# Optimization experiments

Hardware: AMD Instinct MI355X
Metric: run time of the kernel (lower is better)

The kernel has to match this reference:

```python
import jax, jax.numpy as jnp
import numpy as np

D_MODEL = 768
N_HEAD = 12
N_KV_HEADS = 4
HEAD_DIM = D_MODEL // N_HEAD
N_REPEAT = N_HEAD // N_KV_HEADS
ROPE_BASE = 10000.0


def _rotate_half(x):
    # Faithful to the torch impl: reshape(..., 2, d/2) -> transpose(-2,-1) -> reshape
    # (interleaves the two halves), then chunk and cat(-x2, x1).
    d = x.shape[-1]
    xh = x.reshape(*x.shape[:-1], 2, d // 2).swapaxes(-2, -1).reshape(x.shape)
    x1, x2 = jnp.split(xh, 2, axis=-1)
    return jnp.concatenate([-x2, x1], axis=-1)


def _rope(x, pos):
    # x: [B, h, T, d], pos: [T] int
    d = x.shape[-1]
    inv_freq = 1.0 / (ROPE_BASE ** (jnp.arange(0, d, 2, dtype=jnp.float32) / d))
    freqs = pos.astype(jnp.float32)[:, None] * inv_freq[None, :]      # [T, d/2]
    emb = jnp.concatenate([freqs, freqs], axis=-1)                     # [T, d]
    cos = jnp.cos(emb)[None, None]                                     # [1,1,T,d]
    sin = jnp.sin(emb)[None, None]
    xf = x.astype(jnp.float32)
    return (xf * cos + _rotate_half(xf) * sin).astype(x.dtype)


def setup_inputs() -> dict:
    key = jax.random.key(0)
    ks = jax.random.split(key, 6)
    B, T, C = 8, 1024, D_MODEL
    s = 0.02
    return {
        "x": jax.random.normal(ks[0], (B, T, C), dtype=jnp.float32),
        "pos": jnp.arange(T, dtype=jnp.int32),
        "q_w": jax.random.normal(ks[1], (C, N_HEAD * HEAD_DIM), dtype=jnp.float32) * s,
        "q_b": jnp.zeros((N_HEAD * HEAD_DIM,), dtype=jnp.float32),
        "k_w": jax.random.normal(ks[2], (C, N_KV_HEADS * HEAD_DIM), dtype=jnp.float32) * s,
        "k_b": jnp.zeros((N_KV_HEADS * HEAD_DIM,), dtype=jnp.float32),
        "v_w": jax.random.normal(ks[3], (C, N_KV_HEADS * HEAD_DIM), dtype=jnp.float32) * s,
        "v_b": jnp.zeros((N_KV_HEADS * HEAD_DIM,), dtype=jnp.float32),
        "o_w": jax.random.normal(ks[4], (C, C), dtype=jnp.float32) * s,
        "o_b": jnp.zeros((C,), dtype=jnp.float32),
    }


def reference(x, pos, q_w, q_b, k_w, k_b, v_w, v_b, o_w, o_b):
    B, T, C = x.shape
    hd, H, KVH, rep = HEAD_DIM, N_HEAD, N_KV_HEADS, N_REPEAT

    Q = (x @ q_w + q_b).reshape(B, T, H, hd).transpose(0, 2, 1, 3)     # [B,H,T,hd]
    K = (x @ k_w + k_b).reshape(B, T, KVH, hd).transpose(0, 2, 1, 3)   # [B,KVH,T,hd]
    V = (x @ v_w + v_b).reshape(B, T, KVH, hd).transpose(0, 2, 1, 3)

    Q = _rope(Q, pos)
    K = _rope(K, pos)

    # Grouped attention: avoid materializing repeated KV (equiv. to repeat_interleave).
    Qg = Q.reshape(B, KVH, rep, T, hd)
    scores = jnp.einsum("bgrtd,bgsd->bgrts", Qg, K) / np.sqrt(hd).astype(np.float32)
    causal = jnp.tril(jnp.ones((T, T), dtype=bool))
    scores = jnp.where(causal, scores, jnp.finfo(scores.dtype).min)
    probs = jax.nn.softmax(scores, axis=-1)
    out = jnp.einsum("bgrts,bgsd->bgrtd", probs, V)                    # [B,KVH,rep,T,hd]
    out = out.reshape(B, H, T, hd).transpose(0, 2, 1, 3).reshape(B, T, C)
    return out @ o_w + o_b
```

## Files before the change

kernel.cpp:

```cpp
#include <hip/hip_runtime.h>
#include <hip/hip_bf16.h>
#include <math.h>

#define BATCH 8
#define SEQ   1024
#define DM    768
#define NHEAD 12
#define KVH   4
#define HD    64
#define REP   3

#define QSCALE 0.18033688011112042f

typedef unsigned short u16;
typedef __attribute__((ext_vector_type(8))) __bf16 bf16x8;
typedef __attribute__((ext_vector_type(4))) float f32x4;
typedef __attribute__((ext_vector_type(4))) unsigned int u32x4;
typedef __attribute__((address_space(1))) const unsigned int gu32_c;
typedef __attribute__((address_space(3))) unsigned int su32;

__device__ __forceinline__ u16 f2bf(float f) {
    unsigned int u = __float_as_uint(f);
    u += 0x7fffu + ((u >> 16) & 1u);
    return (u16)(u >> 16);
}

__global__ __launch_bounds__(256) void cvt_x_k(
    const float* __restrict__ in, u16* __restrict__ o, int n4)
{
    const int i = blockIdx.x * 256 + threadIdx.x;
    if (i >= n4) return;
    const float4 v = ((const float4*)in)[i];
    ushort4 r;
    r.x = f2bf(v.x); r.y = f2bf(v.y); r.z = f2bf(v.z); r.w = f2bf(v.w);
    ((ushort4*)o)[i] = r;
}

__global__ __launch_bounds__(256) void cvt_wqkv_k(
    const float* __restrict__ qw, const float* __restrict__ kw,
    const float* __restrict__ vw, u16* __restrict__ wt)
{
    const int idx = blockIdx.x * 256 + threadIdx.x;
    if (idx >= 1280 * DM) return;
    const int k = idx % DM;
    const int n = idx / DM;
    float v;
    if (n < 768)       v = qw[(size_t)k * 768 + n] * QSCALE;
    else if (n < 1024) v = kw[(size_t)k * 256 + (n - 768)];
    else               v = vw[(size_t)k * 256 + (n - 1024)];
    wt[idx] = f2bf(v);
}

__global__ __launch_bounds__(256) void cvt_wo_k(
    const float* __restrict__ ow, u16* __restrict__ wt)
{
    const int idx = blockIdx.x * 256 + threadIdx.x;
    if (idx >= DM * DM) return;
    const int k = idx % DM;
    const int n = idx / DM;
    wt[idx] = f2bf(ow[(size_t)k * DM + n]);
}

__device__ __forceinline__ void gemm128_body(
    const u16* __restrict__ A, const u16* __restrict__ B,
    int m0, int n0, u16 (*As)[4096], u16 (*Bs)[4096], f32x4 acc[4][4])
{
    const int tid  = threadIdx.x;
    const int lane = tid & 63;
    const int wid  = tid >> 6;
    const int wr = wid >> 1, wc = wid & 1;
    const int lo = lane & 15, hi = lane >> 4;

    const f32x4 z = {0.f, 0.f, 0.f, 0.f};
    #pragma unroll
    for (int i = 0; i < 4; i++)
        #pragma unroll
        for (int j = 0; j < 4; j++)
            acc[i][j] = z;

    const int NT = DM / 32;

    #define STAGE_G(kt_, sl_) do {                                            \
        _Pragma("unroll")                                                     \
        for (int r_ = 0; r_ < 2; ++r_) {                                      \
            const int idx_  = r_ * 256 + tid;                                 \
            const int row_  = idx_ >> 2;                                      \
            const int col_  = (idx_ & 3) << 3;                                \
            const int base_ = (r_ * 256 + wid * 64) * 8;                      \
            __builtin_amdgcn_global_load_lds(                                 \
                (gu32_c*)&A[(size_t)(m0 + row_) * DM + (kt_) * 32 + col_],    \
                (su32*)&As[sl_][base_], 16, 0, 0);                            \
            __builtin_amdgcn_global_load_lds(                                 \
                (gu32_c*)&B[(size_t)(n0 + row_) * DM + (kt_) * 32 + col_],    \
                (su32*)&Bs[sl_][base_], 16, 0, 0);                            \
        }                                                                     \
    } while (0)

    STAGE_G(0, 0);
    STAGE_G(1, 1);

    for (int kt = 0; kt < NT; ++kt) {
        const int k2 = (kt + 2 < NT) ? kt + 2 : NT - 1;
        STAGE_G(k2, (kt + 2) & 3);
        asm volatile("s_waitcnt vmcnt(8)" ::: "memory");
        __builtin_amdgcn_s_barrier();
        __builtin_amdgcn_sched_barrier(0);

        const int sl = kt & 3;
        bf16x8 af[4], bfr[4];
        #pragma unroll
        for (int i = 0; i < 4; i++) af[i]  = *(const bf16x8*)&As[sl][(wr * 64 + i * 16 + lo) * 32 + hi * 8];
        #pragma unroll
        for (int j = 0; j < 4; j++) bfr[j] = *(const bf16x8*)&Bs[sl][(wc * 64 + j * 16 + lo) * 32 + hi * 8];
        #pragma unroll
        for (int i = 0; i < 4; i++)
            #pragma unroll
            for (int j = 0; j < 4; j++)
                acc[i][j] = __builtin_amdgcn_mfma_f32_16x16x32_bf16(af[i], bfr[j], acc[i][j], 0, 0, 0);
    }
    #undef STAGE_G
}

__global__ __launch_bounds__(256) void gemm_qkv(
    const u16* __restrict__ xb, const u16* __restrict__ wt,
    const float* __restrict__ qb, const float* __restrict__ kb,
    const float* __restrict__ vb,
    u16* __restrict__ Q, u16* __restrict__ K, u16* __restrict__ Vr)
{
    __shared__ __align__(16) u16 As[4][4096];
    __shared__ __align__(16) u16 Bs[4][4096];
    const int id = (blockIdx.x & 7) * 80 + (blockIdx.x >> 3);
    const int m0 = (id / 10) * 128;
    const int n0 = (id % 10) * 128;
    f32x4 acc[4][4];
    gemm128_body(xb, wt, m0, n0, As, Bs, acc);

    const int tid = threadIdx.x;
    const int lane = tid & 63, wid = tid >> 6;
    const int wr = wid >> 1, wc = wid & 1;
    const int lo = lane & 15, hi = lane >> 4;

    #pragma unroll
    for (int j = 0; j < 4; j++) {
        const int n = n0 + wc * 64 + j * 16 + lo;
        u16* outp; int nl, Hcnt; float bias;
        if (n < 768)       { outp = Q;  nl = n;        Hcnt = NHEAD; bias = qb[n] * QSCALE; }
        else if (n < 1024) { outp = K;  nl = n - 768;  Hcnt = KVH;   bias = kb[nl]; }
        else               { outp = Vr; nl = n - 1024; Hcnt = KVH;   bias = vb[nl]; }
        const int head = nl >> 6, d = nl & 63;
        #pragma unroll
        for (int i = 0; i < 4; i++) {
            #pragma unroll
            for (int r = 0; r < 4; r++) {
                const int m = m0 + wr * 64 + i * 16 + hi * 4 + r;
                const int b = m >> 10, t = m & 1023;
                outp[(((size_t)(b * Hcnt + head)) * SEQ + t) * HD + d] =
                    f2bf(acc[i][j][r] + bias);
            }
        }
    }
}

__global__ __launch_bounds__(256) void vtrans_k(
    const u16* __restrict__ in, u16* __restrict__ out)
{
    __shared__ u16 T[64][72];
    const int blk = blockIdx.x;
    const int bg  = blk >> 4;
    const int t0  = (blk & 15) << 6;
    const int tid = threadIdx.x;
    const int tl  = tid & 63;
    const int d0  = (tid >> 6) << 4;

    union { u32x4 v[2]; u16 u[16]; } ld;
    const u16* src = in + ((size_t)bg * SEQ + t0 + tl) * HD + d0;
    ld.v[0] = *(const u32x4*)(src);
    ld.v[1] = *(const u32x4*)(src + 8);
    #pragma unroll
    for (int k = 0; k < 16; ++k) T[d0 + k][tl] = ld.u[k];
    __syncthreads();

    const int d  = tid >> 2;
    const int tc = (tid & 3) << 4;
    u16* dst = out + ((size_t)bg * HD + d) * SEQ + t0 + tc;
    *(u32x4*)(dst)     = *(const u32x4*)&T[d][tc];
    *(u32x4*)(dst + 8) = *(const u32x4*)&T[d][tc + 8];
}

__global__ __launch_bounds__(256) void gemm_oproj(
    const u16* __restrict__ Ab, const u16* __restrict__ wt,
    const float* __restrict__ ob, float* __restrict__ outp)
{
    __shared__ __align__(16) u16 As[4][4096];
    __shared__ __align__(16) u16 Bs[4][4096];
    const int id = (blockIdx.x & 7) * 48 + (blockIdx.x >> 3);
    const int m0 = (id / 6) * 128;
    const int n0 = (id % 6) * 128;
    f32x4 acc[4][4];
    gemm128_body(Ab, wt, m0, n0, As, Bs, acc);

    const int tid = threadIdx.x;
    const int lane = tid & 63, wid = tid >> 6;
    const int wr = wid >> 1, wc = wid & 1;
    const int lo = lane & 15, hi = lane >> 4;

    #pragma unroll
    for (int j = 0; j < 4; j++) {
        const int n = n0 + wc * 64 + j * 16 + lo;
        const float bias = ob[n];
        #pragma unroll
        for (int i = 0; i < 4; i++) {
            #pragma unroll
            for (int r = 0; r < 4; r++) {
                const int m = m0 + wr * 64 + i * 16 + hi * 4 + r;
                outp[(size_t)m * DM + n] = acc[i][j][r] + bias;
            }
        }
    }
}

__global__ __launch_bounds__(256) void rope_naive(
    const __hip_bfloat16* __restrict__ Qin, __hip_bfloat16* __restrict__ Qout,
    const __hip_bfloat16* __restrict__ Kin, __hip_bfloat16* __restrict__ Kout,
    const int* __restrict__ pos)
{
    const long long qrows = (long long)BATCH * NHEAD * SEQ;
    const long long krows = (long long)BATCH * KVH * SEQ;
    const long long gid = (long long)blockIdx.x * 256 + threadIdx.x;
    if (gid >= (qrows + krows) * 64) return;
    long long row = gid >> 6;
    const int j = (int)(gid & 63);
    const __hip_bfloat16* in; __hip_bfloat16* outb;
    if (row < qrows) { in = Qin; outb = Qout; }
    else             { in = Kin; outb = Kout; row -= qrows; }
    const int t = (int)(row & (SEQ - 1));

    float p;
    if (pos[1] == 1)                              p = (float)pos[t];
    else if (((const float*)pos)[1] == 1.0f)      p = ((const float*)pos)[t];
    else                                          p = (float)pos[2 * t];

    const float inv = exp2f(-(float)(j & 31) * (13.287712379549449f / 32.0f));
    float sv, cv;
    sincosf(p * inv, &sv, &cv);
    const int partner = (j & 1) * 32 + (j >> 1) + ((j < 32) ? 16 : -16);
    const float sign  = (j < 32) ? -1.0f : 1.0f;
    const float val  = __bfloat162float(in[row * HD + j]);
    const float pv   = __bfloat162float(in[row * HD + partner]);
    outb[row * HD + j] = __float2bfloat16(val * cv + sign * pv * sv);
}

__device__ __forceinline__ void strip_compute(
    const bf16x8& qf0, const bf16x8& qf1,
    const bf16x8& k0, const bf16x8& k1, const bf16x8& k2, const bf16x8& k3,
    const bf16x8* vv, bool diag, int msk0, int hi,
    float& m, float& l, f32x4* O)
{
    const f32x4 z = {0.f, 0.f, 0.f, 0.f};
    f32x4 a0 = z, a1 = z;
    __builtin_amdgcn_s_setprio(1);
    a0 = __builtin_amdgcn_mfma_f32_16x16x32_bf16(k0, qf0, a0, 0, 0, 0);
    a0 = __builtin_amdgcn_mfma_f32_16x16x32_bf16(k1, qf1, a0, 0, 0, 0);
    a1 = __builtin_amdgcn_mfma_f32_16x16x32_bf16(k2, qf0, a1, 0, 0, 0);
    a1 = __builtin_amdgcn_mfma_f32_16x16x32_bf16(k3, qf1, a1, 0, 0, 0);
    __builtin_amdgcn_s_setprio(0);

    float sc[8];
    #pragma unroll
    for (int e = 0; e < 8; ++e)
        sc[e] = (e < 4) ? a0[e & 3] : a1[e & 3];
    if (diag) {
        #pragma unroll
        for (int e = 0; e < 8; ++e) {
            const int srel = ((e >> 2) << 4) + (hi << 2) + (e & 3);
            if (srel > msk0) sc[e] = -3.0e38f;
        }
    }
    float pm = sc[0];
    #pragma unroll
    for (int e = 1; e < 8; ++e) pm = fmaxf(pm, sc[e]);

    if (!__all(pm - m <= 8.0f)) {
        float pr = fmaxf(pm, __shfl_xor(pm, 16));
        pr = fmaxf(pr, __shfl_xor(pr, 32));
        const float mn = fmaxf(m, pr);
        const float f = exp2f(m - mn);
        l *= f;
        #pragma unroll
        for (int r = 0; r < 4; ++r) {
            const float fr = __shfl(f, hi * 4 + r);
            #pragma unroll
            for (int dj = 0; dj < 4; ++dj) O[dj][r] *= fr;
        }
        m = mn;
    }

    union { u16 u[8]; bf16x8 v; } pu;
    float ps = 0.f;
    #pragma unroll
    for (int e = 0; e < 8; ++e) {
        const float p = exp2f(sc[e] - m);
        ps += p;
        pu.u[e] = f2bf(p);
    }
    l += ps;

    __builtin_amdgcn_s_setprio(1);
    #pragma unroll
    for (int dj = 0; dj < 4; ++dj)
        O[dj] = __builtin_amdgcn_mfma_f32_16x16x32_bf16(pu.v, vv[dj], O[dj], 0, 0, 0);
    __builtin_amdgcn_s_setprio(0);
}

__global__ __launch_bounds__(256, 2) void attn_mfma(
    const u16* __restrict__ Q, const u16* __restrict__ K,
    const u16* __restrict__ Vt, u16* __restrict__ outp)
{
    __shared__ __align__(16) u16 Ks[4][2048];
    __shared__ __align__(16) u16 Vs[4][2048];

    const int wg = (blockIdx.x & 7) * 96 + (blockIdx.x >> 3);
    const int bh = wg >> 3;
    const int c  = wg & 7;
    const int b  = bh / NHEAD, h = bh % NHEAD;
    const int g  = h / REP;
    const int wid  = threadIdx.x >> 6;
    const int lane = threadIdx.x & 63;
    const int lo = lane & 15, hi = lane >> 4;

    const int w    = c + (wid << 3);
    const int sA   = 63 - w, sB = w;
    const int dA   = sA >> 1, dB = sB >> 1;
    const int mskA = lo + ((sA & 1) << 4);
    const int mskB = lo + ((sB & 1) << 4);
    const int nstT = ((63 - c) >> 1) + 1;

    const u16* Kp = K  + (size_t)(b * KVH + g) * SEQ * HD;
    const u16* Vp = Vt + (size_t)(b * KVH + g) * SEQ * HD;

    const int jK = (wid << 6) + lane;
    const int sKoff = (jK ^ ((jK >> 3) & 7)) << 3;
    int vsoff[4];
    #pragma unroll
    for (int q = 0; q < 4; ++q) {
        const int dw  = (wid << 8) + (q << 6) + lane;
        const int R   = dw >> 4;
        const int wd  = dw & 15;
        const int hpl = (wd >> 2) ^ ((R >> 1) & 3);
        vsoff[q] = (R << 10) + (hpl << 2) + (((wd >> 1) & 1) << 4) + ((wd & 1) << 1);
    }

    const u16* QpA = Q + ((size_t)(b * NHEAD + h) * SEQ + (sA << 4)) * HD;
    const u16* QpB = Q + ((size_t)(b * NHEAD + h) * SEQ + (sB << 4)) * HD;
    const bf16x8 qA0 = *(const bf16x8*)&QpA[(size_t)lo * HD + hi * 8];
    const bf16x8 qA1 = *(const bf16x8*)&QpA[(size_t)lo * HD + 32 + hi * 8];
    const bf16x8 qB0 = *(const bf16x8*)&QpB[(size_t)lo * HD + hi * 8];
    const bf16x8 qB1 = *(const bf16x8*)&QpB[(size_t)lo * HD + 32 + hi * 8];

    const f32x4 z = {0.f, 0.f, 0.f, 0.f};
    f32x4 OA[4], OB[4];
    #pragma unroll
    for (int dj = 0; dj < 4; ++dj) { OA[dj] = z; OB[dj] = z; }
    float mA = -3.0e38f, lA = 0.f, mB = -3.0e38f, lB = 0.f;

    #define STAGE(st_, sl_) do {                                              \
        const int s0_ = (st_) << 5;                                           \
        __builtin_amdgcn_global_load_lds(                                     \
            (gu32_c*)(Kp + (s0_ << 6) + sKoff),                               \
            (su32*)&Ks[sl_][wid << 9], 16, 0, 0);                             \
        _Pragma("unroll")                                                     \
        for (int q_ = 0; q_ < 4; ++q_)                                        \
            __builtin_amdgcn_global_load_lds(                                 \
                (gu32_c*)(Vp + s0_ + vsoff[q_]),                              \
                (su32*)&Vs[sl_][(wid << 9) + (q_ << 7)], 4, 0, 0);            \
    } while (0)

    STAGE(0, 0);
    STAGE(1, 1);

    const int xorK = lo & 7;
    for (int st = 0; st < nstT; ++st) {
        const int s2 = (st + 2 < nstT) ? st + 2 : nstT - 1;
        STAGE(s2, (st + 2) & 3);
        asm volatile("s_waitcnt vmcnt(10)" ::: "memory");
        __builtin_amdgcn_s_barrier();
        __builtin_amdgcn_sched_barrier(0);

        if (st <= dA) {
            const int sl = st & 3;
            const u16* kb_ = Ks[sl];
            const bf16x8 k0 = *(const bf16x8*)&kb_[((lo << 3) + (hi ^ xorK)) << 3];
            const bf16x8 k1 = *(const bf16x8*)&kb_[((lo << 3) + ((4 + hi) ^ xorK)) << 3];
            const bf16x8 k2 = *(const bf16x8*)&kb_[(((16 + lo) << 3) + (hi ^ xorK)) << 3];
            const bf16x8 k3 = *(const bf16x8*)&kb_[(((16 + lo) << 3) + ((4 + hi) ^ xorK)) << 3];
            bf16x8 vv[4];
            #pragma unroll
            for (int dj = 0; dj < 4; ++dj) {
                const int R = dj * 16 + lo;
                vv[dj] = *(const bf16x8*)&Vs[sl][(R << 5) + ((hi ^ ((R >> 1) & 3)) << 3)];
            }
            strip_compute(qA0, qA1, k0, k1, k2, k3, vv, st == dA, mskA, hi, mA, lA, OA);
            if (st <= dB)
                strip_compute(qB0, qB1, k0, k1, k2, k3, vv, st == dB, mskB, hi, mB, lB, OB);
        }
    }
    #undef STAGE

    lA += __shfl_xor(lA, 16); lA += __shfl_xor(lA, 32);
    lB += __shfl_xor(lB, 16); lB += __shfl_xor(lB, 32);
    #pragma unroll
    for (int r = 0; r < 4; ++r) {
        const float liA = 1.0f / fmaxf(__shfl(lA, hi * 4 + r), 1e-37f);
        const float liB = 1.0f / fmaxf(__shfl(lB, hi * 4 + r), 1e-37f);
        const int tA = (sA << 4) + hi * 4 + r;
        const int tB = (sB << 4) + hi * 4 + r;
        #pragma unroll
        for (int dj = 0; dj < 4; ++dj) {
            outp[((size_t)(b * SEQ + tA)) * DM + h * HD + dj * 16 + lo] = f2bf(OA[dj][r] * liA);
            outp[((size_t)(b * SEQ + tB)) * DM + h * HD + dj * 16 + lo] = f2bf(OB[dj][r] * liB);
        }
    }
}

extern "C" void kernel_launch(void* const* d_in, const int* in_sizes, int n_in,
                              void* d_out, int out_size, void* d_ws, size_t ws_size,
                              hipStream_t stream) {
    const float* x   = (const float*)d_in[0];
    const int*   pos = (const int*)d_in[1];
    const float* qw  = (const float*)d_in[2];
    const float* qb  = (const float*)d_in[3];
    const float* kw  = (const float*)d_in[4];
    const float* kb  = (const float*)d_in[5];
    const float* vw  = (const float*)d_in[6];
    const float* vb  = (const float*)d_in[7];
    const float* ow  = (const float*)d_in[8];
    const float* ob  = (const float*)d_in[9];
    float* out = (float*)d_out;

    u16* xb    = (u16*)d_ws;
    u16* Wqkvt = xb    + (size_t)8192 * DM;
    u16* Wot   = Wqkvt + (size_t)1280 * DM;
    u16* Qbuf  = Wot   + (size_t)DM * DM;
    u16* Kbuf  = Qbuf  + (size_t)BATCH * NHEAD * SEQ * HD;
    u16* Krot  = Kbuf  + (size_t)BATCH * KVH * SEQ * HD;
    u16* Vtb   = Krot  + (size_t)BATCH * KVH * SEQ * HD;
    u16* Qrot  = xb;
    u16* attn  = Qbuf;
    u16* Vraw  = Krot;

    cvt_x_k<<<(8192 * DM / 4 + 255) / 256, 256, 0, stream>>>(x, xb, 8192 * DM / 4);
    cvt_wqkv_k<<<(1280 * DM + 255) / 256, 256, 0, stream>>>(qw, kw, vw, Wqkvt);
    cvt_wo_k<<<(DM * DM + 255) / 256, 256, 0, stream>>>(ow, Wot);

    gemm_qkv<<<640, 256, 0, stream>>>(xb, Wqkvt, qb, kb, vb, Qbuf, Kbuf, Vraw);

    vtrans_k<<<512, 256, 0, stream>>>(Vraw, Vtb);

    const long long allrows = (long long)BATCH * (NHEAD + KVH) * SEQ;
    rope_naive<<<(int)((allrows * 64 + 255) / 256), 256, 0, stream>>>(
        (const __hip_bfloat16*)Qbuf, (__hip_bfloat16*)Qrot,
        (const __hip_bfloat16*)Kbuf, (__hip_bfloat16*)Krot, pos);

    attn_mfma<<<96 * 8, 256, 0, stream>>>(Qrot, Krot, Vtb, attn);

    gemm_oproj<<<384, 256, 0, stream>>>(attn, Wot, ob, out);
}
```

Before: 229.8 us.

## Split attention blocks to one strip per wave and fuse conversion kernels

The attention kernel now gives each wave a single 16-row query strip instead of a paired long/short strip. This doubles the grid to 1536 blocks, raises launch bounds to 4 blocks per CU, and orders blocks longest-first, with each XCD grouped by batch and KV head for K/V cache reuse. Separately, the three fp32-to-bf16 conversion kernels are merged into one launch. The gain sought is more occupancy and less launch overhead. The cost is that blocks now have uneven causal work and there are fewer accumulators per wave to hide latency.

```diff
diff --git a/kernel.cpp b/kernel.cpp
--- a/kernel.cpp
+++ b/kernel.cpp
@@ -25,40 +25,36 @@
     return (u16)(u >> 16);
 }
 
-__global__ __launch_bounds__(256) void cvt_x_k(
-    const float* __restrict__ in, u16* __restrict__ o, int n4)
-{
+__global__ __launch_bounds__(256) void cvt_all(
+    const float* __restrict__ x,
+    const float* __restrict__ qw, const float* __restrict__ kw,
+    const float* __restrict__ vw, const float* __restrict__ ow,
+    u16* __restrict__ xb, u16* __restrict__ wqkvt, u16* __restrict__ wot)
+{
+    const int NX = 8192 * DM / 4;
+    const int NW = 1280 * DM;
+    const int NO = DM * DM;
     const int i = blockIdx.x * 256 + threadIdx.x;
-    if (i >= n4) return;
-    const float4 v = ((const float4*)in)[i];
-    ushort4 r;
-    r.x = f2bf(v.x); r.y = f2bf(v.y); r.z = f2bf(v.z); r.w = f2bf(v.w);
-    ((ushort4*)o)[i] = r;
-}
-
-__global__ __launch_bounds__(256) void cvt_wqkv_k(
-    const float* __restrict__ qw, const float* __restrict__ kw,
-    const float* __restrict__ vw, u16* __restrict__ wt)
-{
-    const int idx = blockIdx.x * 256 + threadIdx.x;
-    if (idx >= 1280 * DM) return;
-    const int k = idx % DM;
-    const int n = idx / DM;
-    float v;
-    if (n < 768)       v = qw[(size_t)k * 768 + n] * QSCALE;
-    else if (n < 1024) v = kw[(size_t)k * 256 + (n - 768)];
-    else               v = vw[(size_t)k * 256 + (n - 1024)];
-    wt[idx] = f2bf(v);
-}
-
-__global__ __launch_bounds__(256) void cvt_wo_k(
-    const float* __restrict__ ow, u16* __restrict__ wt)
-{
-    const int idx = blockIdx.x * 256 + threadIdx.x;
-    if (idx >= DM * DM) return;
-    const int k = idx % DM;
-    const int n = idx / DM;
-    wt[idx] = f2bf(ow[(size_t)k * DM + n]);
+    if (i < NX) {
+        const float4 v = ((const float4*)x)[i];
+        ushort4 r;
+        r.x = f2bf(v.x); r.y = f2bf(v.y); r.z = f2bf(v.z); r.w = f2bf(v.w);
+        ((ushort4*)xb)[i] = r;
+    } else if (i < NX + NW) {
+        const int idx = i - NX;
+        const int k = idx % DM;
+        const int n = idx / DM;
+        float v;
+        if (n < 768)       v = qw[(size_t)k * 768 + n] * QSCALE;
+        else if (n < 1024) v = kw[(size_t)k * 256 + (n - 768)];
+        else               v = vw[(size_t)k * 256 + (n - 1024)];
+        wqkvt[idx] = f2bf(v);
+    } else if (i < NX + NW + NO) {
+        const int idx = i - NX - NW;
+        const int k = idx % DM;
+        const int n = idx / DM;
+        wot[idx] = f2bf(ow[(size_t)k * DM + n]);
+    }
 }
 
 __device__ __forceinline__ void gemm128_body(
@@ -312,28 +308,32 @@
     __builtin_amdgcn_s_setprio(0);
 }
 
-__global__ __launch_bounds__(256, 2) void attn_mfma(
+__global__ __launch_bounds__(256, 4) void attn_mfma(
     const u16* __restrict__ Q, const u16* __restrict__ K,
     const u16* __restrict__ Vt, u16* __restrict__ outp)
 {
     __shared__ __align__(16) u16 Ks[4][2048];
     __shared__ __align__(16) u16 Vs[4][2048];
 
-    const int wg = (blockIdx.x & 7) * 96 + (blockIdx.x >> 3);
-    const int bh = wg >> 3;
-    const int c  = wg & 7;
-    const int b  = bh / NHEAD, h = bh % NHEAD;
-    const int g  = h / REP;
+    const int blk = blockIdx.x;
+    const int xcd = blk & 7;
+    const int jj  = blk >> 3;
+    const int bg  = (xcd << 2) + (jj & 3);
+    const int rh  = jj >> 2;
+    const int a   = 15 - rh / 3;
+    const int hl  = rh % 3;
+    const int b   = bg >> 2, g = bg & 3;
+    const int h   = g * REP + hl;
+
     const int wid  = threadIdx.x >> 6;
     const int lane = threadIdx.x & 63;
     const int lo = lane & 15, hi = lane >> 4;
 
-    const int w    = c + (wid << 3);
-    const int sA   = 63 - w, sB = w;
-    const int dA   = sA >> 1, dB = sB >> 1;
-    const int mskA = lo + ((sA & 1) << 4);
-    const int mskB = lo + ((sB & 1) << 4);
-    const int nstT = ((63 - c) >> 1) + 1;
+    const int w    = (a << 2) + wid;
+    const int q0   = w << 4;
+    const int dT   = w >> 1;
+    const int msk0 = lo + ((w & 1) << 4);
+    const int nstT = (a << 1) + 2;
 
     const u16* Kp = K  + (size_t)(b * KVH + g) * SEQ * HD;
     const u16* Vp = Vt + (size_t)(b * KVH + g) * SEQ * HD;
@@ -350,18 +350,15 @@
         vsoff[q] = (R << 10) + (hpl << 2) + (((wd >> 1) & 1) << 4) + ((wd & 1) << 1);
     }
 
-    const u16* QpA = Q + ((size_t)(b * NHEAD + h) * SEQ + (sA << 4)) * HD;
-    const u16* QpB = Q + ((size_t)(b * NHEAD + h) * SEQ + (sB << 4)) * HD;
-    const bf16x8 qA0 = *(const bf16x8*)&QpA[(size_t)lo * HD + hi * 8];
-    const bf16x8 qA1 = *(const bf16x8*)&QpA[(size_t)lo * HD + 32 + hi * 8];
-    const bf16x8 qB0 = *(const bf16x8*)&QpB[(size_t)lo * HD + hi * 8];
-    const bf16x8 qB1 = *(const bf16x8*)&QpB[(size_t)lo * HD + 32 + hi * 8];
+    const u16* Qp = Q + ((size_t)(b * NHEAD + h) * SEQ + q0) * HD;
+    const bf16x8 qf0 = *(const bf16x8*)&Qp[(size_t)lo * HD + hi * 8];
+    const bf16x8 qf1 = *(const bf16x8*)&Qp[(size_t)lo * HD + 32 + hi * 8];
 
     const f32x4 z = {0.f, 0.f, 0.f, 0.f};
-    f32x4 OA[4], OB[4];
-    #pragma unroll
-    for (int dj = 0; dj < 4; ++dj) { OA[dj] = z; OB[dj] = z; }
-    float mA = -3.0e38f, lA = 0.f, mB = -3.0e38f, lB = 0.f;
+    f32x4 O[4];
+    #pragma unroll
+    for (int dj = 0; dj < 4; ++dj) O[dj] = z;
+    float m = -3.0e38f, l = 0.f;
 
     #define STAGE(st_, sl_) do {                                              \
         const int s0_ = (st_) << 5;                                           \
@@ -386,7 +383,7 @@
         __builtin_amdgcn_s_barrier();
         __builtin_amdgcn_sched_barrier(0);
 
-        if (st <= dA) {
+        if (st <= dT) {
             const int sl = st & 3;
             const u16* kb_ = Ks[sl];
             const bf16x8 k0 = *(const bf16x8*)&kb_[((lo << 3) + (hi ^ xorK)) << 3];
@@ -399,26 +396,19 @@
                 const int R = dj * 16 + lo;
                 vv[dj] = *(const bf16x8*)&Vs[sl][(R << 5) + ((hi ^ ((R >> 1) & 3)) << 3)];
             }
-            strip_compute(qA0, qA1, k0, k1, k2, k3, vv, st == dA, mskA, hi, mA, lA, OA);
-            if (st <= dB)
-                strip_compute(qB0, qB1, k0, k1, k2, k3, vv, st == dB, mskB, hi, mB, lB, OB);
+            strip_compute(qf0, qf1, k0, k1, k2, k3, vv, st == dT, msk0, hi, m, l, O);
         }
     }
     #undef STAGE
 
-    lA += __shfl_xor(lA, 16); lA += __shfl_xor(lA, 32);
-    lB += __shfl_xor(lB, 16); lB += __shfl_xor(lB, 32);
+    l += __shfl_xor(l, 16); l += __shfl_xor(l, 32);
     #pragma unroll
     for (int r = 0; r < 4; ++r) {
-        const float liA = 1.0f / fmaxf(__shfl(lA, hi * 4 + r), 1e-37f);
-        const float liB = 1.0f / fmaxf(__shfl(lB, hi * 4 + r), 1e-37f);
-        const int tA = (sA << 4) + hi * 4 + r;
-        const int tB = (sB << 4) + hi * 4 + r;
-        #pragma unroll
-        for (int dj = 0; dj < 4; ++dj) {
-            outp[((size_t)(b * SEQ + tA)) * DM + h * HD + dj * 16 + lo] = f2bf(OA[dj][r] * liA);
-            outp[((size_t)(b * SEQ + tB)) * DM + h * HD + dj * 16 + lo] = f2bf(OB[dj][r] * liB);
-        }
+        const float li = 1.0f / fmaxf(__shfl(l, hi * 4 + r), 1e-37f);
+        const int t = q0 + hi * 4 + r;
+        #pragma unroll
+        for (int dj = 0; dj < 4; ++dj)
+            outp[((size_t)(b * SEQ + t)) * DM + h * HD + dj * 16 + lo] = f2bf(O[dj][r] * li);
     }
 }
 
@@ -448,9 +438,8 @@
     u16* attn  = Qbuf;
     u16* Vraw  = Krot;
 
-    cvt_x_k<<<(8192 * DM / 4 + 255) / 256, 256, 0, stream>>>(x, xb, 8192 * DM / 4);
-    cvt_wqkv_k<<<(1280 * DM + 255) / 256, 256, 0, stream>>>(qw, kw, vw, Wqkvt);
-    cvt_wo_k<<<(DM * DM + 255) / 256, 256, 0, stream>>>(ow, Wot);
+    const int NCVT = 8192 * DM / 4 + 1280 * DM + DM * DM;
+    cvt_all<<<(NCVT + 255) / 256, 256, 0, stream>>>(x, qw, kw, vw, ow, xb, Wqkvt, Wot);
 
     gemm_qkv<<<640, 256, 0, stream>>>(xb, Wqkvt, qb, kb, vb, Qbuf, Kbuf, Vraw);
 
@@ -461,7 +450,7 @@
         (const __hip_bfloat16*)Qbuf, (__hip_bfloat16*)Qrot,
         (const __hip_bfloat16*)Kbuf, (__hip_bfloat16*)Krot, pos);
 
-    attn_mfma<<<96 * 8, 256, 0, stream>>>(Qrot, Krot, Vtb, attn);
+    attn_mfma<<<1536, 256, 0, stream>>>(Qrot, Krot, Vtb, attn);
 
     gemm_oproj<<<384, 256, 0, stream>>>(attn, Wot, ob, out);
 }
```

New measurement: 215.1 us. 6.4% less time.
